# Optimization experiments

Hardware: AMD Instinct MI355X
Metric: run time of the kernel (lower is better)

Reference implementation:

```python
import jax, jax.numpy as jnp
import numpy as np

NUM_NODES = 100000   # KG entity count (embedding table)
N_SUB = 20000        # subgraph nodes
E = 400000           # edges
R = 16               # num_rels
B = 8                # num_bases (block-diagonal decomposition)
H = 256              # h_dim (submat = H // B = 32)
PAIRS = 4096         # DTI drug-target pairs


def _rgcn_bdd_layer(x, src, dst, etype, norm, W, loop_w, bias):
    """DGL RelGraphConv with 'bdd' regularizer, self_loop=True, activation=None.

    message_e = blockdiag(W[etype_e]) @ x[src_e] * norm_e ; out_v = sum_e->v message_e
    By linearity we first segment-sum norm-scaled source features per (dst, rel)
    bucket, then apply the R relation block transforms once per node -- same math,
    no per-edge weight gather.
    """
    N, h = x.shape
    si = h // B  # block input size == block output size here
    contrib = x[src] * norm                      # [E, H]
    seg = dst * R + etype                        # bucket per (dst node, relation)
    agg = jax.ops.segment_sum(contrib, seg, num_segments=N * R)
    agg = agg.reshape(N, R, B, si)               # [N, R, B, si]
    msg = jnp.einsum('nrbi,rbio->nbo', agg, W).reshape(N, h)
    return msg + bias + x @ loop_w               # self-loop + bias (activation=None)


def setup_inputs() -> dict:
    key = jax.random.key(0)
    ks = jax.random.split(key, 20)
    si = H // B
    inp = {
        'drugs_index': jax.random.randint(ks[0], (PAIRS,), 0, N_SUB, dtype=jnp.int32),
        'targets_index': jax.random.randint(ks[1], (PAIRS,), 0, N_SUB, dtype=jnp.int32),
        'node_ids': jax.random.randint(ks[2], (N_SUB,), 0, NUM_NODES, dtype=jnp.int32),
        'src': jax.random.randint(ks[3], (E,), 0, N_SUB, dtype=jnp.int32),
        'dst': jax.random.randint(ks[4], (E,), 0, N_SUB, dtype=jnp.int32),
        'etype': jax.random.randint(ks[5], (E,), 0, R, dtype=jnp.int32),
        'norm': jax.random.uniform(ks[6], (E, 1), dtype=jnp.float32),
    }
    s_h = 1.0 / np.sqrt(H)
    s_blk = 1.0 / np.sqrt(si)
    inp['emb'] = jax.random.normal(ks[7], (NUM_NODES, H), jnp.float32)
    inp['w1'] = jax.random.normal(ks[8], (R, B, si, si), jnp.float32) * s_blk
    inp['loop_w1'] = jax.random.normal(ks[9], (H, H), jnp.float32) * s_h
    inp['b1'] = jnp.zeros((H,), jnp.float32)
    inp['w2'] = jax.random.normal(ks[10], (R, B, si, si), jnp.float32) * s_blk
    inp['loop_w2'] = jax.random.normal(ks[11], (H, H), jnp.float32) * s_h
    inp['b2'] = jnp.zeros((H,), jnp.float32)
    d = 2 * H
    inp['fc1_W'] = jax.random.normal(ks[12], (d, d), jnp.float32) / np.sqrt(d)
    inp['fc1_b'] = jnp.zeros((d,), jnp.float32)
    inp['fc2_W'] = jax.random.normal(ks[13], (d, 1), jnp.float32) / np.sqrt(d)
    inp['fc2_b'] = jnp.zeros((1,), jnp.float32)
    return inp


def reference(drugs_index, targets_index, node_ids, src, dst, etype, norm,
              emb, w1, loop_w1, b1, w2, loop_w2, b2,
              fc1_W, fc1_b, fc2_W, fc2_b):
    h = emb[node_ids]                                      # EmbeddingLayer
    h = _rgcn_bdd_layer(h, src, dst, etype, norm, w1, loop_w1, b1)
    h = _rgcn_bdd_layer(h, src, dst, etype, norm, w2, loop_w2, b2)
    x = jnp.concatenate([h[drugs_index], h[targets_index]], axis=1)  # [PAIRS, 2H]
    x = jax.nn.relu(x @ fc1_W + fc1_b)                     # dropout=0 -> identity
    return jax.nn.sigmoid(x @ fc2_W + fc2_b)               # [PAIRS, 1]
```

## Files before the change

### kernel.cpp

```cpp
#include <hip/hip_runtime.h>
#include <math.h>

typedef __attribute__((ext_vector_type(8))) short short8;
typedef __attribute__((ext_vector_type(4))) float f32x4;

#define N_SUBN   20000
#define E_EDGES  400000
#define R_REL    16
#define H_DIM    256
#define NBINS    (N_SUBN * R_REL)
#define SCAN_CHUNK 2048
#define NSCAN_BLOCKS ((NBINS + SCAN_CHUNK - 1) / SCAN_CHUNK)
#define NPAIRS   4096
#define TILE_N   32
#define NT_BLOCKS (N_SUBN / TILE_N)
#define D2       512

__device__ __forceinline__ ushort f2bf(float x) {
    uint u = __float_as_uint(x);
    u += 0x7fffu + ((u >> 16) & 1u);
    return (ushort)(u >> 16);
}
__device__ __forceinline__ float bf2f(ushort h) {
    return __uint_as_float(((uint)h) << 16);
}

__global__ void k_gather(const float* __restrict__ emb, const int* __restrict__ nid,
                         float* __restrict__ h0) {
    int t = blockIdx.x * blockDim.x + threadIdx.x;
    int node = t >> 6, c = (t & 63) << 2;
    if (node >= N_SUBN) return;
    const float4 s = *reinterpret_cast<const float4*>(emb + (size_t)nid[node] * H_DIM + c);
    *reinterpret_cast<float4*>(h0 + (size_t)node * H_DIM + c) = s;
}

__global__ void k_count(const int* __restrict__ dst, const int* __restrict__ ety,
                        int* __restrict__ cnt) {
    int e = blockIdx.x * 256 + threadIdx.x;
    if (e < E_EDGES) atomicAdd(&cnt[dst[e] * R_REL + ety[e]], 1);
}

__global__ void k_scan1(int* __restrict__ data, int* __restrict__ bs) {
    __shared__ int ts[256];
    int base = blockIdx.x * SCAN_CHUNK + threadIdx.x * 8;
    int v[8]; int s = 0;
#pragma unroll
    for (int j = 0; j < 8; j++) {
        int idx = base + j;
        v[j] = (idx < NBINS) ? data[idx] : 0;
        s += v[j];
    }
    ts[threadIdx.x] = s;
    __syncthreads();
    for (int off = 1; off < 256; off <<= 1) {
        int add = (threadIdx.x >= (unsigned)off) ? ts[threadIdx.x - off] : 0;
        __syncthreads();
        ts[threadIdx.x] += add;
        __syncthreads();
    }
    int excl = ts[threadIdx.x] - s;
    if (threadIdx.x == 255) bs[blockIdx.x] = ts[255];
    int run = excl;
#pragma unroll
    for (int j = 0; j < 8; j++) {
        int idx = base + j;
        if (idx < NBINS) data[idx] = run;
        run += v[j];
    }
}

__global__ void k_scan2(int* __restrict__ bs) {
    __shared__ int ls[NSCAN_BLOCKS];
    if (threadIdx.x < NSCAN_BLOCKS) ls[threadIdx.x] = bs[threadIdx.x];
    __syncthreads();
    if (threadIdx.x == 0) {
        int run = 0;
        for (int i = 0; i < NSCAN_BLOCKS; i++) { int t = ls[i]; ls[i] = run; run += t; }
    }
    __syncthreads();
    if (threadIdx.x < NSCAN_BLOCKS) bs[threadIdx.x] = ls[threadIdx.x];
}

__global__ void k_scan3(int* __restrict__ data, const int* __restrict__ bs) {
    int idx = blockIdx.x * 256 + threadIdx.x;
    if (idx < NBINS) data[idx] = data[idx] + bs[idx / SCAN_CHUNK];
}

__global__ void k_scatter(const int* __restrict__ src, const int* __restrict__ dst,
                          const int* __restrict__ ety, const float* __restrict__ nrm,
                          int* __restrict__ segend, uint* __restrict__ es) {
    int e = blockIdx.x * 256 + threadIdx.x;
    if (e >= E_EDGES) return;
    int bin = dst[e] * R_REL + ety[e];
    int pos = atomicAdd(&segend[bin], 1);
    float n = nrm[e];
    uint q = (uint)fminf(n * 131072.f + 0.5f, 131071.f);
    es[pos] = ((uint)src[e] << 17) | q;
}

__global__ void k_prep_w(const float* __restrict__ w, ushort* __restrict__ wfrag) {
    int t = blockIdx.x * 256 + threadIdx.x;
    int lane = t & 63, f = t >> 6;
    int ot = f & 1, rb = f >> 1;
    int kbase = (lane >> 4) * 8, n = ot * 16 + (lane & 15);
    ushort hv[8], lv[8];
#pragma unroll
    for (int j = 0; j < 8; j++) {
        float x = w[(size_t)(rb * 32 + kbase + j) * 32 + n];
        ushort h = f2bf(x);
        ushort l = f2bf(x - bf2f(h));
        hv[j] = h; lv[j] = l;
    }
    *reinterpret_cast<short8*>(wfrag + ((size_t)(f * 2 + 0) * 64 + lane) * 8) =
        *reinterpret_cast<short8*>(hv);
    *reinterpret_cast<short8*>(wfrag + ((size_t)(f * 2 + 1) * 64 + lane) * 8) =
        *reinterpret_cast<short8*>(lv);
}

__global__ void k_prep_lw(const float* __restrict__ lw, ushort* __restrict__ lwfrag) {
    int t = blockIdx.x * 256 + threadIdx.x;
    int lane = t & 63, g = t >> 6;
    int kt = g >> 4, ot = g & 15;
    int kbase = kt * 32 + (lane >> 4) * 8, n = ot * 16 + (lane & 15);
    ushort hv[8], lv[8];
#pragma unroll
    for (int j = 0; j < 8; j++) {
        float x = lw[(size_t)(kbase + j) * H_DIM + n];
        ushort h = f2bf(x);
        ushort l = f2bf(x - bf2f(h));
        hv[j] = h; lv[j] = l;
    }
    *reinterpret_cast<short8*>(lwfrag + ((size_t)(g * 2 + 0) * 64 + lane) * 8) =
        *reinterpret_cast<short8*>(hv);
    *reinterpret_cast<short8*>(lwfrag + ((size_t)(g * 2 + 1) * 64 + lane) * 8) =
        *reinterpret_cast<short8*>(lv);
}

__global__ void k_prep_fc1(const float* __restrict__ w, ushort* __restrict__ wfrag) {
    int t = blockIdx.x * 256 + threadIdx.x;
    int lane = t & 63, g = t >> 6;
    int kt = g >> 5, ot = g & 31;
    int kbase = kt * 32 + (lane >> 4) * 8, n = ot * 16 + (lane & 15);
    ushort hv[8], lv[8];
#pragma unroll
    for (int j = 0; j < 8; j++) {
        float x = w[(size_t)(kbase + j) * D2 + n];
        ushort h = f2bf(x);
        ushort l = f2bf(x - bf2f(h));
        hv[j] = h; lv[j] = l;
    }
    *reinterpret_cast<short8*>(wfrag + ((size_t)(g * 2 + 0) * 64 + lane) * 8) =
        *reinterpret_cast<short8*>(hv);
    *reinterpret_cast<short8*>(wfrag + ((size_t)(g * 2 + 1) * 64 + lane) * 8) =
        *reinterpret_cast<short8*>(lv);
}

__global__ __launch_bounds__(512) void k_layer(
    const float* __restrict__ hin, const uint* __restrict__ es, const int* __restrict__ segend,
    const ushort* __restrict__ wfrag, const ushort* __restrict__ lwfrag,
    const float* __restrict__ bias, float* __restrict__ hout) {
    __shared__ __align__(16) ushort aggH[TILE_N * H_DIM];
    __shared__ __align__(16) ushort aggLo[TILE_N * H_DIM];
    __shared__ int lofs[TILE_N * R_REL + 1];
    char* cH = (char*)aggH;
    char* cL = (char*)aggLo;
    const int n0 = blockIdx.x * TILE_N;
    const int tid = threadIdx.x;
    const int lane = tid & 63, wv = tid >> 6;
    const int col = lane & 15, kg = lane >> 4;
    const short8* wf  = (const short8*)wfrag;
    const short8* lwf = (const short8*)lwfrag;

    {
        const int base = n0 * R_REL;
        for (int j = tid; j < TILE_N * R_REL + 1; j += 512) {
            int g = base + j - 1;
            lofs[j] = (g < 0) ? 0 : segend[g];
        }
    }

    f32x4 acc[2][2];
#pragma unroll
    for (int mt = 0; mt < 2; ++mt)
#pragma unroll
        for (int ot = 0; ot < 2; ++ot) acc[mt][ot] = (f32x4){0.f, 0.f, 0.f, 0.f};

    const uint laneoff = (uint)(lane << 2);
    const int t0 = 4 * wv;

    for (int r = 0; r < R_REL; ++r) {
        __syncthreads();
        int e0 = lofs[(t0 + 0) * R_REL + r], d0 = lofs[(t0 + 0) * R_REL + r + 1];
        int e1 = lofs[(t0 + 1) * R_REL + r], d1 = lofs[(t0 + 1) * R_REL + r + 1];
        int e2 = lofs[(t0 + 2) * R_REL + r], d2 = lofs[(t0 + 2) * R_REL + r + 1];
        int e3 = lofs[(t0 + 3) * R_REL + r], d3 = lofs[(t0 + 3) * R_REL + r + 1];
        float4 a0 = make_float4(0.f, 0.f, 0.f, 0.f);
        float4 a1 = make_float4(0.f, 0.f, 0.f, 0.f);
        float4 a2 = make_float4(0.f, 0.f, 0.f, 0.f);
        float4 a3 = make_float4(0.f, 0.f, 0.f, 0.f);
        while ((e0 < d0) | (e1 < d1) | (e2 < d2) | (e3 < d3)) {
            bool g0 = e0 < d0, g1 = e1 < d1, g2 = e2 < d2, g3 = e3 < d3;
            uint p0 = 0, p1 = 0, p2 = 0, p3 = 0;
            if (g0) p0 = es[e0++];
            if (g1) p1 = es[e1++];
            if (g2) p2 = es[e2++];
            if (g3) p3 = es[e3++];
            if (g0) {
                const float4 x = *reinterpret_cast<const float4*>(
                    hin + (size_t)(p0 >> 17) * H_DIM + laneoff);
                float nm = (float)(p0 & 0x1FFFFu) * (1.f / 131072.f);
                a0.x = fmaf(x.x, nm, a0.x); a0.y = fmaf(x.y, nm, a0.y);
                a0.z = fmaf(x.z, nm, a0.z); a0.w = fmaf(x.w, nm, a0.w);
            }
            if (g1) {
                const float4 x = *reinterpret_cast<const float4*>(
                    hin + (size_t)(p1 >> 17) * H_DIM + laneoff);
                float nm = (float)(p1 & 0x1FFFFu) * (1.f / 131072.f);
                a1.x = fmaf(x.x, nm, a1.x); a1.y = fmaf(x.y, nm, a1.y);
                a1.z = fmaf(x.z, nm, a1.z); a1.w = fmaf(x.w, nm, a1.w);
            }
            if (g2) {
                const float4 x = *reinterpret_cast<const float4*>(
                    hin + (size_t)(p2 >> 17) * H_DIM + laneoff);
                float nm = (float)(p2 & 0x1FFFFu) * (1.f / 131072.f);
                a2.x = fmaf(x.x, nm, a2.x); a2.y = fmaf(x.y, nm, a2.y);
                a2.z = fmaf(x.z, nm, a2.z); a2.w = fmaf(x.w, nm, a2.w);
            }
            if (g3) {
                const float4 x = *reinterpret_cast<const float4*>(
                    hin + (size_t)(p3 >> 17) * H_DIM + laneoff);
                float nm = (float)(p3 & 0x1FFFFu) * (1.f / 131072.f);
                a3.x = fmaf(x.x, nm, a3.x); a3.y = fmaf(x.y, nm, a3.y);
                a3.z = fmaf(x.z, nm, a3.z); a3.w = fmaf(x.w, nm, a3.w);
            }
        }
#pragma unroll
        for (int i = 0; i < 4; ++i) {
            float4 av = (i == 0) ? a0 : (i == 1) ? a1 : (i == 2) ? a2 : a3;
            int t = t0 + i;
            ushort h0 = f2bf(av.x), h1 = f2bf(av.y), h2 = f2bf(av.z), h3 = f2bf(av.w);
            uint2 ph = make_uint2((uint)h0 | ((uint)h1 << 16), (uint)h2 | ((uint)h3 << 16));
            uint2 pl = make_uint2(
                (uint)f2bf(av.x - bf2f(h0)) | ((uint)f2bf(av.y - bf2f(h1)) << 16),
                (uint)f2bf(av.z - bf2f(h2)) | ((uint)f2bf(av.w - bf2f(h3)) << 16));
            uint byte = (uint)(t * 512) + ((((lane >> 1) ^ (t & 7)) << 4) | ((lane & 1) << 3));
            *(uint2*)(cH + byte) = ph;
            *(uint2*)(cL + byte) = pl;
        }
        __syncthreads();
#pragma unroll
        for (int ot = 0; ot < 2; ++ot) {
            int f = (r * 8 + wv) * 2 + ot;
            short8 Bh = wf[(f * 2 + 0) * 64 + lane];
            short8 Bl = wf[(f * 2 + 1) * 64 + lane];
#pragma unroll
            for (int mt = 0; mt < 2; ++mt) {
                int row = mt * 16 + col;
                uint ab = (uint)(row * 512) + ((uint)((wv * 4 + kg) ^ (row & 7)) << 4);
                short8 Ah = *(const short8*)(cH + ab);
                short8 Al = *(const short8*)(cL + ab);
                f32x4 a = acc[mt][ot];
                a = __builtin_amdgcn_mfma_f32_16x16x32_bf16(Ah, Bh, a, 0, 0, 0);
                a = __builtin_amdgcn_mfma_f32_16x16x32_bf16(Ah, Bl, a, 0, 0, 0);
                a = __builtin_amdgcn_mfma_f32_16x16x32_bf16(Al, Bh, a, 0, 0, 0);
                acc[mt][ot] = a;
            }
        }
    }

    __syncthreads();
#pragma unroll
    for (int i = 0; i < 4; ++i) {
        int t = t0 + i;
        const float4 xv = *reinterpret_cast<const float4*>(
            hin + (size_t)(n0 + t) * H_DIM + laneoff);
        ushort h0 = f2bf(xv.x), h1 = f2bf(xv.y), h2 = f2bf(xv.z), h3 = f2bf(xv.w);
        uint2 ph = make_uint2((uint)h0 | ((uint)h1 << 16), (uint)h2 | ((uint)h3 << 16));
        uint2 pl = make_uint2(
            (uint)f2bf(xv.x - bf2f(h0)) | ((uint)f2bf(xv.y - bf2f(h1)) << 16),
            (uint)f2bf(xv.z - bf2f(h2)) | ((uint)f2bf(xv.w - bf2f(h3)) << 16));
        uint byte = (uint)(t * 512) + ((((lane >> 1) ^ (t & 7)) << 4) | ((lane & 1) << 3));
        *(uint2*)(cH + byte) = ph;
        *(uint2*)(cL + byte) = pl;
    }
    __syncthreads();
#pragma unroll
    for (int kt = 0; kt < 8; ++kt) {
#pragma unroll
        for (int ot = 0; ot < 2; ++ot) {
            int g = kt * 16 + 2 * wv + ot;
            short8 Bh = lwf[(g * 2 + 0) * 64 + lane];
            short8 Bl = lwf[(g * 2 + 1) * 64 + lane];
#pragma unroll
            for (int mt = 0; mt < 2; ++mt) {
                int row = mt * 16 + col;
                uint ab = (uint)(row * 512) + ((uint)((kt * 4 + kg) ^ (row & 7)) << 4);
                short8 Ah = *(const short8*)(cH + ab);
                short8 Al = *(const short8*)(cL + ab);
                f32x4 a = acc[mt][ot];
                a = __builtin_amdgcn_mfma_f32_16x16x32_bf16(Ah, Bh, a, 0, 0, 0);
                a = __builtin_amdgcn_mfma_f32_16x16x32_bf16(Ah, Bl, a, 0, 0, 0);
                a = __builtin_amdgcn_mfma_f32_16x16x32_bf16(Al, Bh, a, 0, 0, 0);
                acc[mt][ot] = a;
            }
        }
    }

#pragma unroll
    for (int mt = 0; mt < 2; ++mt) {
        int nbase = n0 + mt * 16 + kg * 4;
#pragma unroll
        for (int ot = 0; ot < 2; ++ot) {
            int o = 32 * wv + ot * 16 + col;
            float bo = bias[o];
#pragma unroll
            for (int rg = 0; rg < 4; ++rg)
                hout[(size_t)(nbase + rg) * H_DIM + o] = acc[mt][ot][rg] + bo;
        }
    }
}

__global__ __launch_bounds__(512) void k_mlp(
    const float* __restrict__ h, const int* __restrict__ drugs, const int* __restrict__ targets,
    const ushort* __restrict__ fc1frag, const float* __restrict__ b1f,
    const float* __restrict__ W2, const float* __restrict__ b2f,
    float* __restrict__ outp) {
    __shared__ __align__(16) ushort xH[16 * D2];
    __shared__ __align__(16) ushort xL[16 * D2];
    __shared__ float red[16][8];
    char* cH = (char*)xH;
    char* cL = (char*)xL;
    const int tid = threadIdx.x;
    const int lane = tid & 63, wv = tid >> 6;
    const int col = lane & 15, kg = lane >> 4;
    const int p0 = blockIdx.x * 16;
    const short8* wf = (const short8*)fc1frag;

    {
        int p = tid >> 5;
        int cc = (tid & 31) * 16;
        int di = drugs[p0 + p], ti = targets[p0 + p];
        const float* srcp = (cc < H_DIM) ? (h + (size_t)di * H_DIM + cc)
                                         : (h + (size_t)ti * H_DIM + (cc - H_DIM));
#pragma unroll
        for (int j = 0; j < 2; ++j) {
            float4 a = *reinterpret_cast<const float4*>(srcp + j * 8);
            float4 b = *reinterpret_cast<const float4*>(srcp + j * 8 + 4);
            float f[8] = {a.x, a.y, a.z, a.w, b.x, b.y, b.z, b.w};
            short8 hv, lv;
#pragma unroll
            for (int q = 0; q < 8; ++q) {
                ushort hh = f2bf(f[q]);
                hv[q] = (short)hh;
                lv[q] = (short)f2bf(f[q] - bf2f(hh));
            }
            uint chunk = (uint)((tid & 31) * 2 + j);
            uint byte = (uint)p * 1024 + ((chunk ^ (uint)(p & 7)) << 4);
            *(short8*)(cH + byte) = hv;
            *(short8*)(cL + byte) = lv;
        }
    }
    __syncthreads();

    f32x4 acc[4];
#pragma unroll
    for (int oi = 0; oi < 4; ++oi) acc[oi] = (f32x4){0.f, 0.f, 0.f, 0.f};

    for (int kt = 0; kt < 16; ++kt) {
        uint ab = (uint)col * 1024 + ((uint)((kt * 4 + kg) ^ (col & 7)) << 4);
        short8 Ah = *(const short8*)(cH + ab);
        short8 Al = *(const short8*)(cL + ab);
#pragma unroll
        for (int oi = 0; oi < 4; ++oi) {
            int g = kt * 32 + wv * 4 + oi;
            short8 Bh = wf[(g * 2 + 0) * 64 + lane];
            short8 Bl = wf[(g * 2 + 1) * 64 + lane];
            f32x4 a = acc[oi];
            a = __builtin_amdgcn_mfma_f32_16x16x32_bf16(Ah, Bh, a, 0, 0, 0);
            a = __builtin_amdgcn_mfma_f32_16x16x32_bf16(Ah, Bl, a, 0, 0, 0);
            a = __builtin_amdgcn_mfma_f32_16x16x32_bf16(Al, Bh, a, 0, 0, 0);
            a = __builtin_amdgcn_mfma_f32_16x16x32_bf16(Al, Bl, a, 0, 0, 0);
            acc[oi] = a;
        }
    }

    float val[4] = {0.f, 0.f, 0.f, 0.f};
#pragma unroll
    for (int oi = 0; oi < 4; ++oi) {
        int o = 64 * wv + oi * 16 + col;
        float b1o = b1f[o], w2o = W2[o];
#pragma unroll
        for (int rg = 0; rg < 4; ++rg) {
            float y = acc[oi][rg] + b1o;
            y = y > 0.f ? y : 0.f;
            val[rg] = fmaf(y, w2o, val[rg]);
        }
    }
#pragma unroll
    for (int rg = 0; rg < 4; ++rg) {
        float v = val[rg];
        v += __shfl_xor(v, 1, 64);
        v += __shfl_xor(v, 2, 64);
        v += __shfl_xor(v, 4, 64);
        v += __shfl_xor(v, 8, 64);
        val[rg] = v;
    }
    if (col == 0) {
#pragma unroll
        for (int rg = 0; rg < 4; ++rg) red[kg * 4 + rg][wv] = val[rg];
    }
    __syncthreads();
    if (tid < 16) {
        float s = 0.f;
#pragma unroll
        for (int w = 0; w < 8; w++) s += red[tid][w];
        s += b2f[0];
        outp[p0 + tid] = 1.f / (1.f + __expf(-s));
    }
}

extern "C" void kernel_launch(void* const* d_in, const int* in_sizes, int n_in,
                              void* d_out, int out_size, void* d_ws, size_t ws_size,
                              hipStream_t stream) {
    (void)in_sizes; (void)n_in; (void)out_size; (void)ws_size;
    const int*   drugs   = (const int*)d_in[0];
    const int*   targets = (const int*)d_in[1];
    const int*   nid     = (const int*)d_in[2];
    const int*   src     = (const int*)d_in[3];
    const int*   dst     = (const int*)d_in[4];
    const int*   ety     = (const int*)d_in[5];
    const float* nrm     = (const float*)d_in[6];
    const float* emb     = (const float*)d_in[7];
    const float* w1      = (const float*)d_in[8];
    const float* lw1     = (const float*)d_in[9];
    const float* b1      = (const float*)d_in[10];
    const float* w2      = (const float*)d_in[11];
    const float* lw2     = (const float*)d_in[12];
    const float* b2      = (const float*)d_in[13];
    const float* fc1W    = (const float*)d_in[14];
    const float* fc1b    = (const float*)d_in[15];
    const float* fc2W    = (const float*)d_in[16];
    const float* fc2b    = (const float*)d_in[17];
    float* outp = (float*)d_out;

    char* ws = (char*)d_ws;
    ushort* wfrag1  = (ushort*)(ws);
    ushort* wfrag2  = (ushort*)(ws + 524288);
    ushort* lwfrag1 = (ushort*)(ws + 1048576);
    ushort* lwfrag2 = (ushort*)(ws + 1310720);
    ushort* fc1frag = (ushort*)(ws + 1572864);
    float*  hA      = (float*) (ws + 2621440);
    float*  hB      = (float*) (ws + 23101440);
    int*    segend  = (int*)   (ws + 43581440);
    int*    bs      = (int*)   (ws + 44861440);
    uint*   es      = (uint*)  (ws + 44862464);

    hipMemsetAsync(segend, 0, NBINS * sizeof(int), stream);
    k_prep_w  <<<64, 256, 0, stream>>>(w1, wfrag1);
    k_prep_w  <<<64, 256, 0, stream>>>(w2, wfrag2);
    k_prep_lw <<<32, 256, 0, stream>>>(lw1, lwfrag1);
    k_prep_lw <<<32, 256, 0, stream>>>(lw2, lwfrag2);
    k_prep_fc1<<<128, 256, 0, stream>>>(fc1W, fc1frag);
    k_gather <<<5000, 256, 0, stream>>>(emb, nid, hA);
    k_count  <<<(E_EDGES + 255) / 256, 256, 0, stream>>>(dst, ety, segend);
    k_scan1  <<<NSCAN_BLOCKS, 256, 0, stream>>>(segend, bs);
    k_scan2  <<<1, 256, 0, stream>>>(bs);
    k_scan3  <<<(NBINS + 255) / 256, 256, 0, stream>>>(segend, bs);
    k_scatter<<<(E_EDGES + 255) / 256, 256, 0, stream>>>(src, dst, ety, nrm, segend, es);
    k_layer  <<<NT_BLOCKS, 512, 0, stream>>>(hA, es, segend, wfrag1, lwfrag1, b1, hB);
    k_layer  <<<NT_BLOCKS, 512, 0, stream>>>(hB, es, segend, wfrag2, lwfrag2, b2, hA);
    k_mlp    <<<NPAIRS / 16, 512, 0, stream>>>(hA, drugs, targets, fc1frag, fc1b, fc2W, fc2b, outp);
}
```

Before: 304.0 us.

## Double-buffer per-relation aggregation with MFMA and merge prep kernels plus memset

The layer kernel now keeps two LDS buffers for the bf16 hi/lo aggregate. It computes relation r+1's gather-aggregate while the MFMAs for relation r run, with s_setprio raising priority on the MFMA phases. This drops one barrier per relation and lets the irregular gather latency overlap with matrix math. The cost is double the LDS (64KB per block), which may reduce occupancy. Separately, the five weight-prep kernels and the segend memset are fused into a single launch to cut launch overhead.

```diff
diff --git a/kernel.cpp b/kernel.cpp
--- a/kernel.cpp
+++ b/kernel.cpp
@@ -15,6 +15,7 @@
 #define TILE_N   32
 #define NT_BLOCKS (N_SUBN / TILE_N)
 #define D2       512
+#define PLANE_B  (TILE_N * H_DIM * 2)
 
 __device__ __forceinline__ ushort f2bf(float x) {
     uint u = __float_as_uint(x);
@@ -98,8 +99,8 @@
     es[pos] = ((uint)src[e] << 17) | q;
 }
 
-__global__ void k_prep_w(const float* __restrict__ w, ushort* __restrict__ wfrag) {
-    int t = blockIdx.x * 256 + threadIdx.x;
+__device__ __forceinline__ void prep_w_body(const float* __restrict__ w,
+                                            ushort* __restrict__ wfrag, int t) {
     int lane = t & 63, f = t >> 6;
     int ot = f & 1, rb = f >> 1;
     int kbase = (lane >> 4) * 8, n = ot * 16 + (lane & 15);
@@ -117,8 +118,8 @@
         *reinterpret_cast<short8*>(lv);
 }
 
-__global__ void k_prep_lw(const float* __restrict__ lw, ushort* __restrict__ lwfrag) {
-    int t = blockIdx.x * 256 + threadIdx.x;
+__device__ __forceinline__ void prep_lw_body(const float* __restrict__ lw,
+                                             ushort* __restrict__ lwfrag, int t) {
     int lane = t & 63, g = t >> 6;
     int kt = g >> 4, ot = g & 15;
     int kbase = kt * 32 + (lane >> 4) * 8, n = ot * 16 + (lane & 15);
@@ -136,8 +137,8 @@
         *reinterpret_cast<short8*>(lv);
 }
 
-__global__ void k_prep_fc1(const float* __restrict__ w, ushort* __restrict__ wfrag) {
-    int t = blockIdx.x * 256 + threadIdx.x;
+__device__ __forceinline__ void prep_fc1_body(const float* __restrict__ w,
+                                              ushort* __restrict__ wfrag, int t) {
     int lane = t & 63, g = t >> 6;
     int kt = g >> 5, ot = g & 31;
     int kbase = kt * 32 + (lane >> 4) * 8, n = ot * 16 + (lane & 15);
@@ -155,12 +156,32 @@
         *reinterpret_cast<short8*>(lv);
 }
 
+#define ZBLOCKS ((NBINS + 255) / 256)
+
+__global__ void k_prep_all(const float* __restrict__ w1, const float* __restrict__ w2,
+                           const float* __restrict__ lw1, const float* __restrict__ lw2,
+                           const float* __restrict__ fc1W,
+                           ushort* __restrict__ wfrag1, ushort* __restrict__ wfrag2,
+                           ushort* __restrict__ lwfrag1, ushort* __restrict__ lwfrag2,
+                           ushort* __restrict__ fc1frag, int* __restrict__ segend) {
+    int b = blockIdx.x, tid = threadIdx.x;
+    if (b < 64)        prep_w_body(w1, wfrag1, b * 256 + tid);
+    else if (b < 128)  prep_w_body(w2, wfrag2, (b - 64) * 256 + tid);
+    else if (b < 160)  prep_lw_body(lw1, lwfrag1, (b - 128) * 256 + tid);
+    else if (b < 192)  prep_lw_body(lw2, lwfrag2, (b - 160) * 256 + tid);
+    else if (b < 320)  prep_fc1_body(fc1W, fc1frag, (b - 192) * 256 + tid);
+    else {
+        int i = (b - 320) * 256 + tid;
+        if (i < NBINS) segend[i] = 0;
+    }
+}
+
 __global__ __launch_bounds__(512) void k_layer(
     const float* __restrict__ hin, const uint* __restrict__ es, const int* __restrict__ segend,
     const ushort* __restrict__ wfrag, const ushort* __restrict__ lwfrag,
     const float* __restrict__ bias, float* __restrict__ hout) {
-    __shared__ __align__(16) ushort aggH[TILE_N * H_DIM];
-    __shared__ __align__(16) ushort aggLo[TILE_N * H_DIM];
+    __shared__ __align__(16) ushort aggH[2][TILE_N * H_DIM];
+    __shared__ __align__(16) ushort aggLo[2][TILE_N * H_DIM];
     __shared__ int lofs[TILE_N * R_REL + 1];
     char* cH = (char*)aggH;
     char* cL = (char*)aggLo;
@@ -170,6 +191,8 @@
     const int col = lane & 15, kg = lane >> 4;
     const short8* wf  = (const short8*)wfrag;
     const short8* lwf = (const short8*)lwfrag;
+    const uint laneoff = (uint)(lane << 2);
+    const int t0 = 4 * wv;
 
     {
         const int base = n0 * R_REL;
@@ -185,15 +208,11 @@
 #pragma unroll
         for (int ot = 0; ot < 2; ++ot) acc[mt][ot] = (f32x4){0.f, 0.f, 0.f, 0.f};
 
-    const uint laneoff = (uint)(lane << 2);
-    const int t0 = 4 * wv;
-
-    for (int r = 0; r < R_REL; ++r) {
-        __syncthreads();
-        int e0 = lofs[(t0 + 0) * R_REL + r], d0 = lofs[(t0 + 0) * R_REL + r + 1];
-        int e1 = lofs[(t0 + 1) * R_REL + r], d1 = lofs[(t0 + 1) * R_REL + r + 1];
-        int e2 = lofs[(t0 + 2) * R_REL + r], d2 = lofs[(t0 + 2) * R_REL + r + 1];
-        int e3 = lofs[(t0 + 3) * R_REL + r], d3 = lofs[(t0 + 3) * R_REL + r + 1];
+    auto aggregate = [&](int rr, int bb) {
+        int e0 = lofs[(t0 + 0) * R_REL + rr], d0 = lofs[(t0 + 0) * R_REL + rr + 1];
+        int e1 = lofs[(t0 + 1) * R_REL + rr], d1 = lofs[(t0 + 1) * R_REL + rr + 1];
+        int e2 = lofs[(t0 + 2) * R_REL + rr], d2 = lofs[(t0 + 2) * R_REL + rr + 1];
+        int e3 = lofs[(t0 + 3) * R_REL + rr], d3 = lofs[(t0 + 3) * R_REL + rr + 1];
         float4 a0 = make_float4(0.f, 0.f, 0.f, 0.f);
         float4 a1 = make_float4(0.f, 0.f, 0.f, 0.f);
         float4 a2 = make_float4(0.f, 0.f, 0.f, 0.f);
@@ -234,6 +253,7 @@
                 a3.z = fmaf(x.z, nm, a3.z); a3.w = fmaf(x.w, nm, a3.w);
             }
         }
+        const uint bbase = (uint)bb * PLANE_B;
 #pragma unroll
         for (int i = 0; i < 4; ++i) {
             float4 av = (i == 0) ? a0 : (i == 1) ? a1 : (i == 2) ? a2 : a3;
@@ -243,11 +263,40 @@
             uint2 pl = make_uint2(
                 (uint)f2bf(av.x - bf2f(h0)) | ((uint)f2bf(av.y - bf2f(h1)) << 16),
                 (uint)f2bf(av.z - bf2f(h2)) | ((uint)f2bf(av.w - bf2f(h3)) << 16));
-            uint byte = (uint)(t * 512) + ((((lane >> 1) ^ (t & 7)) << 4) | ((lane & 1) << 3));
+            uint byte = bbase + (uint)(t * 512) +
+                        ((((lane >> 1) ^ (t & 7)) << 4) | ((lane & 1) << 3));
             *(uint2*)(cH + byte) = ph;
             *(uint2*)(cL + byte) = pl;
         }
-        __syncthreads();
+    };
+
+    auto stage_self = [&](int bb) {
+        const uint bbase = (uint)bb * PLANE_B;
+#pragma unroll
+        for (int i = 0; i < 4; ++i) {
+            int t = t0 + i;
+            const float4 xv = *reinterpret_cast<const float4*>(
+                hin + (size_t)(n0 + t) * H_DIM + laneoff);
+            ushort h0 = f2bf(xv.x), h1 = f2bf(xv.y), h2 = f2bf(xv.z), h3 = f2bf(xv.w);
+            uint2 ph = make_uint2((uint)h0 | ((uint)h1 << 16), (uint)h2 | ((uint)h3 << 16));
+            uint2 pl = make_uint2(
+                (uint)f2bf(xv.x - bf2f(h0)) | ((uint)f2bf(xv.y - bf2f(h1)) << 16),
+                (uint)f2bf(xv.z - bf2f(h2)) | ((uint)f2bf(xv.w - bf2f(h3)) << 16));
+            uint byte = bbase + (uint)(t * 512) +
+                        ((((lane >> 1) ^ (t & 7)) << 4) | ((lane & 1) << 3));
+            *(uint2*)(cH + byte) = ph;
+            *(uint2*)(cL + byte) = pl;
+        }
+    };
+
+    __syncthreads();
+    aggregate(0, 0);
+    __syncthreads();
+
+    for (int r = 0; r < R_REL; ++r) {
+        const int cur = r & 1;
+        const uint bbase = (uint)cur * PLANE_B;
+        __builtin_amdgcn_s_setprio(1);
 #pragma unroll
         for (int ot = 0; ot < 2; ++ot) {
             int f = (r * 8 + wv) * 2 + ot;
@@ -256,7 +305,7 @@
 #pragma unroll
             for (int mt = 0; mt < 2; ++mt) {
                 int row = mt * 16 + col;
-                uint ab = (uint)(row * 512) + ((uint)((wv * 4 + kg) ^ (row & 7)) << 4);
+                uint ab = bbase + (uint)(row * 512) + ((uint)((wv * 4 + kg) ^ (row & 7)) << 4);
                 short8 Ah = *(const short8*)(cH + ab);
                 short8 Al = *(const short8*)(cL + ab);
                 f32x4 a = acc[mt][ot];
@@ -266,24 +315,13 @@
                 acc[mt][ot] = a;
             }
         }
-    }
-
-    __syncthreads();
-#pragma unroll
-    for (int i = 0; i < 4; ++i) {
-        int t = t0 + i;
-        const float4 xv = *reinterpret_cast<const float4*>(
-            hin + (size_t)(n0 + t) * H_DIM + laneoff);
-        ushort h0 = f2bf(xv.x), h1 = f2bf(xv.y), h2 = f2bf(xv.z), h3 = f2bf(xv.w);
-        uint2 ph = make_uint2((uint)h0 | ((uint)h1 << 16), (uint)h2 | ((uint)h3 << 16));
-        uint2 pl = make_uint2(
-            (uint)f2bf(xv.x - bf2f(h0)) | ((uint)f2bf(xv.y - bf2f(h1)) << 16),
-            (uint)f2bf(xv.z - bf2f(h2)) | ((uint)f2bf(xv.w - bf2f(h3)) << 16));
-        uint byte = (uint)(t * 512) + ((((lane >> 1) ^ (t & 7)) << 4) | ((lane & 1) << 3));
-        *(uint2*)(cH + byte) = ph;
-        *(uint2*)(cL + byte) = pl;
-    }
-    __syncthreads();
+        __builtin_amdgcn_s_setprio(0);
+        if (r < R_REL - 1) aggregate(r + 1, cur ^ 1);
+        else               stage_self(cur ^ 1);
+        __syncthreads();
+    }
+
+    __builtin_amdgcn_s_setprio(1);
 #pragma unroll
     for (int kt = 0; kt < 8; ++kt) {
 #pragma unroll
@@ -305,6 +343,7 @@
             }
         }
     }
+    __builtin_amdgcn_s_setprio(0);
 
 #pragma unroll
     for (int mt = 0; mt < 2; ++mt) {
@@ -455,12 +494,9 @@
     int*    bs      = (int*)   (ws + 44861440);
     uint*   es      = (uint*)  (ws + 44862464);
 
-    hipMemsetAsync(segend, 0, NBINS * sizeof(int), stream);
-    k_prep_w  <<<64, 256, 0, stream>>>(w1, wfrag1);
-    k_prep_w  <<<64, 256, 0, stream>>>(w2, wfrag2);
-    k_prep_lw <<<32, 256, 0, stream>>>(lw1, lwfrag1);
-    k_prep_lw <<<32, 256, 0, stream>>>(lw2, lwfrag2);
-    k_prep_fc1<<<128, 256, 0, stream>>>(fc1W, fc1frag);
+    k_prep_all<<<320 + ZBLOCKS, 256, 0, stream>>>(w1, w2, lw1, lw2, fc1W,
+                                                  wfrag1, wfrag2, lwfrag1, lwfrag2,
+                                                  fc1frag, segend);
     k_gather <<<5000, 256, 0, stream>>>(emb, nid, hA);
     k_count  <<<(E_EDGES + 255) / 256, 256, 0, stream>>>(dst, ety, segend);
     k_scan1  <<<NSCAN_BLOCKS, 256, 0, stream>>>(segend, bs);
```

Result: slower. 409.9 us (+34.8%).
